# Performance work log

Measured on AMD Instinct MI355X. Metric: run time of the kernel, lower is better.

The kernel has to match this reference:

```python
import jax, jax.numpy as jnp
import numpy as np

WIN = (8, 8)
N_WIN_TOK = WIN[0] * WIN[1]  # 64
DIM = 128
HEADS = 4
HEAD_DIM = DIM // HEADS
HIDDEN = int(DIM * 0.25)
B_ = 16384


def _relative_position_index():
    ch = np.arange(WIN[0])
    cw = np.arange(WIN[1])
    coords = np.stack(np.meshgrid(ch, cw, indexing='ij'))      # (2, Wh, Ww)
    flat = coords.reshape(2, -1)                                # (2, N)
    rel = flat[:, :, None] - flat[:, None, :]                   # (2, N, N)
    rel = rel.transpose(1, 2, 0).astype(np.int32)               # (N, N, 2)
    rel[:, :, 0] += WIN[0] - 1
    rel[:, :, 1] += WIN[1] - 1
    rel[:, :, 0] *= 2 * WIN[1] - 1
    return jnp.asarray(rel.sum(-1), dtype=jnp.int32)            # (N, N)


def setup_inputs() -> dict:
    key = jax.random.key(0)
    ks = jax.random.split(key, 8)
    s_in = 1.0 / np.sqrt(DIM)
    s_h = 1.0 / np.sqrt(HIDDEN)
    return {
        'x': jax.random.normal(ks[0], (B_, N_WIN_TOK, DIM), jnp.float32),
        'rpb_table': 0.02 * jax.random.normal(ks[1], ((2 * WIN[0] - 1) * (2 * WIN[1] - 1), HEADS), jnp.float32),
        'wq': s_in * jax.random.normal(ks[2], (DIM, DIM), jnp.float32),
        'bq': jnp.zeros((DIM,), jnp.float32),
        'wkv': s_in * jax.random.normal(ks[3], (DIM, 2 * DIM), jnp.float32),
        'bkv': jnp.zeros((2 * DIM,), jnp.float32),
        'fc1_w': s_in * jax.random.normal(ks[4], (DIM, HIDDEN), jnp.float32),
        'fc1_b': jnp.zeros((HIDDEN,), jnp.float32),
        'fc2_w': s_h * jax.random.normal(ks[5], (HIDDEN, DIM), jnp.float32),
        'fc2_b': jnp.zeros((DIM,), jnp.float32),
        'rel_idx': _relative_position_index(),
    }


def reference(x, rpb_table, wq, bq, wkv, bkv, fc1_w, fc1_b, fc2_w, fc2_b, rel_idx):
    B, N, C = x.shape
    scale = HEAD_DIM ** -0.5
    # qkv projections (Uformer LinearProjection): q from to_q, k/v from to_kv
    q = (x @ wq + bq).reshape(B, N, HEADS, HEAD_DIM).transpose(0, 2, 1, 3)   # (B,h,N,d)
    kv = (x @ wkv + bkv).reshape(B, N, 2, HEADS, HEAD_DIM)
    k = kv[:, :, 0].transpose(0, 2, 1, 3)                                    # (B,h,N,d)
    v = kv[:, :, 1].transpose(0, 2, 1, 3)
    attn = jnp.einsum('bhnd,bhmd->bhnm', q * scale, k)                       # (B,h,N,N)
    bias = rpb_table[rel_idx]                                                # (N,N,h)
    attn = attn + bias.transpose(2, 0, 1)[None]                              # + (1,h,N,N)
    attn = jax.nn.softmax(attn, axis=-1)
    out = jnp.einsum('bhnm,bhmd->bhnd', attn, v).transpose(0, 2, 1, 3).reshape(B, N, C)
    # Mlp proj: fc1 -> GELU -> fc2
    out = jax.nn.gelu(out @ fc1_w + fc1_b, approximate=False) @ fc2_w + fc2_b
    return out
```

## Files before the change

### kernel.cpp

```cpp
#include <hip/hip_runtime.h>
#include <hip/hip_bf16.h>
#include <math.h>

typedef __bf16 bf16x8 __attribute__((ext_vector_type(8)));
typedef __bf16 bf16x4 __attribute__((ext_vector_type(4)));
typedef float f32x4 __attribute__((ext_vector_type(4)));

static __device__ __forceinline__ f32x4 mfma16(bf16x8 a, bf16x8 b, f32x4 c) {
  return __builtin_amdgcn_mfma_f32_16x16x32_bf16(a, b, c, 0, 0, 0);
}


__global__ void wattn_prep(const float* __restrict__ wq, const float* __restrict__ bq,
                           const float* __restrict__ wkv,
                           const float* __restrict__ f1w, const float* __restrict__ f2w,
                           const float* __restrict__ rpb, const int* __restrict__ rel,
                           char* __restrict__ ws)
{
  const int idx = blockIdx.x * 256 + threadIdx.x;
  const float scale = 0.17677669529663687f;
  unsigned short* ws16 = (unsigned short*)ws;
  float* wsf = (float*)ws;

  if (idx < 2048) {
    const int lane = idx & 63, dt = (idx >> 6) & 7, kt = idx >> 9;
    const int gg = lane >> 4, cc = lane & 15;
    bf16x8 v;
#pragma unroll
    for (int i = 0; i < 8; ++i)
      v[i] = (__bf16)(wq[(kt * 32 + gg * 8 + i) * 128 + dt * 16 + cc] * scale);
    *(bf16x8*)(ws16 + idx * 8) = v;
  } else if (idx < 4096) {
    const int e = idx - 2048;
    const int lane = e & 63, dt = (e >> 6) & 7, kt = e >> 9;
    const int gg = lane >> 4, cc = lane & 15;
    bf16x8 v;
#pragma unroll
    for (int i = 0; i < 8; ++i)
      v[i] = (__bf16)(wkv[(kt * 32 + gg * 8 + i) * 256 + dt * 16 + cc]);
    *(bf16x8*)(ws16 + 16384 + e * 8) = v;
  } else if (idx < 6144) {
    const int e = idx - 4096;
    const int lane = e & 63, dt = (e >> 6) & 7, kt = e >> 9;
    const int gg = lane >> 4, cc = lane & 15;
    bf16x8 v;
#pragma unroll
    for (int i = 0; i < 8; ++i)
      v[i] = (__bf16)(wkv[(kt * 32 + gg * 8 + i) * 256 + 128 + dt * 16 + cc]);
    *(bf16x8*)(ws16 + 32768 + e * 8) = v;
  } else if (idx < 6656) {
    const int e = idx - 6144;
    const int lane = e & 63, ht = (e >> 6) & 1, kt = e >> 7;
    const int gg = lane >> 4, cc = lane & 15;
    bf16x8 v;
#pragma unroll
    for (int i = 0; i < 8; ++i)
      v[i] = (__bf16)(f1w[(kt * 32 + gg * 8 + i) * 32 + ht * 16 + cc]);
    *(bf16x8*)(ws16 + 49152 + e * 8) = v;
  } else if (idx < 7168) {
    const int e = idx - 6656;
    const int lane = e & 63, dt = e >> 6;
    const int gg = lane >> 4, cc = lane & 15;
    bf16x8 v;
#pragma unroll
    for (int i = 0; i < 8; ++i)
      v[i] = (__bf16)(f2w[(gg * 8 + i) * 128 + dt * 16 + cc]);
    *(bf16x8*)(ws16 + 53248 + e * 8) = v;
  } else if (idx < 11264) {
    const int e = idx - 7168;
    const int lane = e & 63, nt = (e >> 6) & 3, mt = (e >> 8) & 3, h = e >> 10;
    const int gg = lane >> 4, cc = lane & 15;
    const int q = nt * 16 + cc;
    f32x4 v;
#pragma unroll
    for (int r = 0; r < 4; ++r) {
      const int key = mt * 16 + gg * 4 + r;
      v[r] = rpb[rel[q * 64 + key] * 4 + h];
    }
    *(f32x4*)(wsf + 28672 + e * 4) = v;
  } else if (idx < 11392) {
    const int d = idx - 11264;
    wsf[45056 + d] = bq[d] * scale;
  }
}

__global__ __launch_bounds__(256, 2) void wattn_main(
    const float* __restrict__ x,
    const float* __restrict__ bkv,
    const float* __restrict__ f1b,
    const float* __restrict__ f2b,
    const char* __restrict__ ws,
    float* __restrict__ out)
{
  extern __shared__ char smem[];
  const int tid = threadIdx.x;
  const int w = tid >> 6;
  const int l = tid & 63;
  const int g = l >> 4;
  const int c = l & 15;
  const size_t b = blockIdx.x;

  const unsigned short* ws16 = (const unsigned short*)ws;
  const bf16x8* wqp = (const bf16x8*)(ws16);
  const bf16x8* wkp = (const bf16x8*)(ws16 + 16384);
  const bf16x8* wvp = (const bf16x8*)(ws16 + 32768);
  const bf16x8* f1p = (const bf16x8*)(ws16 + 49152);
  const bf16x8* f2p = (const bf16x8*)(ws16 + 53248);
  const f32x4* biasp = (const f32x4*)(ws16 + 57344);
  const float* bqs = (const float*)(ws16 + 90112);

  {
    const float* xg = x + b * 8192;
#pragma unroll
    for (int i = 0; i < 8; ++i) {
      const int idx = i * 256 + tid;
      f32x4 v = *((const f32x4*)xg + idx);
      const int row = idx >> 5;
      const int col = (idx & 31) << 2;
      const int addr = (((row << 8) + (col << 1))) ^ ((row & 7) << 4);
      bf16x4 p = { (__bf16)v[0], (__bf16)v[1], (__bf16)v[2], (__bf16)v[3] };
      *(bf16x4*)(smem + addr) = p;
    }
  }
  __syncthreads();

  bf16x8 xf[4];
  {
    const int row = w * 16 + c;
    const int sw = (row & 7) << 4;
#pragma unroll
    for (int kt = 0; kt < 4; ++kt)
      xf[kt] = *(const bf16x8*)(smem + (((row << 8) + kt * 64 + (g << 4)) ^ sw));
  }
  {
    const int row = w * 16 + c;
    const int sw = (row & 7) << 4;
#pragma unroll
    for (int dt = 0; dt < 8; ++dt) {
      f32x4 aq = *(const f32x4*)(bqs + dt * 16 + g * 4);
      f32x4 ak = *(const f32x4*)(bkv + dt * 16 + g * 4);
#pragma unroll
      for (int kt = 0; kt < 4; ++kt) {
        aq = mfma16(wqp[(kt * 8 + dt) * 64 + l], xf[kt], aq);
        ak = mfma16(wkp[(kt * 8 + dt) * 64 + l], xf[kt], ak);
      }
      const int addr = (((row << 8) + dt * 32 + g * 8)) ^ sw;
      bf16x4 q4 = { (__bf16)aq[0], (__bf16)aq[1], (__bf16)aq[2], (__bf16)aq[3] };
      bf16x4 k4 = { (__bf16)ak[0], (__bf16)ak[1], (__bf16)ak[2], (__bf16)ak[3] };
      *(bf16x4*)(smem + 16384 + addr) = q4;
      *(bf16x4*)(smem + 32768 + addr) = k4;
    }
  }
  {
#pragma unroll
    for (int dt = 0; dt < 8; ++dt) {
      const float bv = bkv[128 + dt * 16 + c];
      f32x4 av = { bv, bv, bv, bv };
#pragma unroll
      for (int kt = 0; kt < 4; ++kt)
        av = mfma16(xf[kt], wvp[(kt * 8 + dt) * 64 + l], av);
      const int row = dt * 16 + c;
      const int addr = (((row << 7) + w * 32 + g * 8)) ^ ((row & 7) << 4);
      bf16x4 v4 = { (__bf16)av[0], (__bf16)av[1], (__bf16)av[2], (__bf16)av[3] };
      *(bf16x4*)(smem + 49152 + addr) = v4;
    }
  }
  __syncthreads();

  bf16x8 ka[4], qb[4];
#pragma unroll
  for (int t4 = 0; t4 < 4; ++t4) {
    const int row = t4 * 16 + c;
    const int addr = (((row << 8) + w * 64 + (g << 4))) ^ ((row & 7) << 4);
    ka[t4] = *(const bf16x8*)(smem + 32768 + addr);
    qb[t4] = *(const bf16x8*)(smem + 16384 + addr);
  }
  f32x4 s[4][4];
#pragma unroll
  for (int mt = 0; mt < 4; ++mt)
#pragma unroll
    for (int nt = 0; nt < 4; ++nt)
      s[mt][nt] = mfma16(ka[mt], qb[nt], biasp[((w * 4 + mt) * 4 + nt) * 64 + l]);
  __syncthreads();

  float rinv[4];
#pragma unroll
  for (int nt = 0; nt < 4; ++nt) {
    float m = s[0][nt][0];
#pragma unroll
    for (int mt = 0; mt < 4; ++mt)
#pragma unroll
      for (int r = 0; r < 4; ++r)
        m = fmaxf(m, s[mt][nt][r]);
    m = fmaxf(m, __shfl_xor(m, 16, 64));
    m = fmaxf(m, __shfl_xor(m, 32, 64));
    float sum = 0.f;
#pragma unroll
    for (int mt = 0; mt < 4; ++mt)
#pragma unroll
      for (int r = 0; r < 4; ++r) {
        const float e = __expf(s[mt][nt][r] - m);
        s[mt][nt][r] = e;
        sum += e;
      }
    sum += __shfl_xor(sum, 16, 64);
    sum += __shfl_xor(sum, 32, 64);
    rinv[nt] = 1.0f / sum;
  }

  const int pbase = (w < 2) ? (w * 8192) : (32768 + (w - 2) * 8192);
#pragma unroll
  for (int nt = 0; nt < 4; ++nt) {
    const int row = nt * 16 + c;
    const int sw = (row & 7) << 4;
#pragma unroll
    for (int mt = 0; mt < 4; ++mt) {
      const int addr = (((row << 7) + mt * 32 + g * 8)) ^ sw;
      bf16x4 p4 = { (__bf16)s[mt][nt][0], (__bf16)s[mt][nt][1],
                    (__bf16)s[mt][nt][2], (__bf16)s[mt][nt][3] };
      *(bf16x4*)(smem + pbase + addr) = p4;
    }
  }

  bf16x8 va[2][2], pbf[2][4];
#pragma unroll
  for (int dt2 = 0; dt2 < 2; ++dt2)
#pragma unroll
    for (int ks = 0; ks < 2; ++ks) {
      const int row = (2 * w + dt2) * 16 + c;
      const int addr = (((row << 7) + ks * 64 + (g << 4))) ^ ((row & 7) << 4);
      va[dt2][ks] = *(const bf16x8*)(smem + 49152 + addr);
    }
#pragma unroll
  for (int ks = 0; ks < 2; ++ks)
#pragma unroll
    for (int nt = 0; nt < 4; ++nt) {
      const int row = nt * 16 + c;
      const int addr = (((row << 7) + ks * 64 + (g << 4))) ^ ((row & 7) << 4);
      pbf[ks][nt] = *(const bf16x8*)(smem + pbase + addr);
    }
#pragma unroll
  for (int nt = 0; nt < 4; ++nt) {
    const int row = nt * 16 + c;
    const int sw = (row & 7) << 4;
    const float rv = rinv[nt];
#pragma unroll
    for (int dt2 = 0; dt2 < 2; ++dt2) {
      f32x4 acc = { 0.f, 0.f, 0.f, 0.f };
      acc = mfma16(va[dt2][0], pbf[0][nt], acc);
      acc = mfma16(va[dt2][1], pbf[1][nt], acc);
      const int addr = (((row << 8) + (2 * w + dt2) * 32 + g * 8)) ^ sw;
      bf16x4 o4 = { (__bf16)(acc[0] * rv), (__bf16)(acc[1] * rv),
                    (__bf16)(acc[2] * rv), (__bf16)(acc[3] * rv) };
      *(bf16x4*)(smem + 16384 + addr) = o4;
    }
  }
  __syncthreads();

  bf16x8 ob[4];
  {
    const int row = w * 16 + c;
    const int sw = (row & 7) << 4;
#pragma unroll
    for (int kt = 0; kt < 4; ++kt)
      ob[kt] = *(const bf16x8*)(smem + 16384 + (((row << 8) + kt * 64 + (g << 4)) ^ sw));
  }
  {
    const int row = w * 16 + c;
    const int sw = (row & 7) << 4;
#pragma unroll
    for (int ht = 0; ht < 2; ++ht) {
      f32x4 ah = *(const f32x4*)(f1b + ht * 16 + g * 4);
#pragma unroll
      for (int kt = 0; kt < 4; ++kt)
        ah = mfma16(f1p[(kt * 2 + ht) * 64 + l], ob[kt], ah);
      bf16x4 h4;
#pragma unroll
      for (int r = 0; r < 4; ++r) {
        const float v = ah[r];
        h4[r] = (__bf16)(0.5f * v * (1.0f + erff(v * 0.70710678118654752f)));
      }
      *(bf16x4*)(smem + 49152 + (((row << 6) + ht * 32 + g * 8) ^ sw)) = h4;
    }
  }
  bf16x8 ha;
  {
    const int row = w * 16 + c;
    ha = *(const bf16x8*)(smem + 49152 + (((row << 6) + (g << 4)) ^ ((row & 7) << 4)));
  }
  {
    float* og = out + b * 8192 + (size_t)(w * 16) * 128;
#pragma unroll
    for (int dt = 0; dt < 8; ++dt) {
      const float bb = f2b[dt * 16 + c];
      f32x4 ay = { bb, bb, bb, bb };
      ay = mfma16(ha, f2p[dt * 64 + l], ay);
#pragma unroll
      for (int r = 0; r < 4; ++r)
        og[(g * 4 + r) * 128 + dt * 16 + c] = ay[r];
    }
  }
}

extern "C" void kernel_launch(void* const* d_in, const int* in_sizes, int n_in,
                              void* d_out, int out_size, void* d_ws, size_t ws_size,
                              hipStream_t stream) {
  const float* x    = (const float*)d_in[0];
  const float* rpb  = (const float*)d_in[1];
  const float* wq   = (const float*)d_in[2];
  const float* bq   = (const float*)d_in[3];
  const float* wkv  = (const float*)d_in[4];
  const float* bkv  = (const float*)d_in[5];
  const float* f1w  = (const float*)d_in[6];
  const float* f1b  = (const float*)d_in[7];
  const float* f2w  = (const float*)d_in[8];
  const float* f2b  = (const float*)d_in[9];
  const int*   rel  = (const int*)d_in[10];
  float* out = (float*)d_out;
  char* ws = (char*)d_ws;
  if (ws_size < 180736) return;

  const int nB = in_sizes[0] / 8192;

  wattn_prep<<<45, 256, 0, stream>>>(wq, bq, wkv, f1w, f2w, rpb, rel, ws);
  wattn_main<<<nB, 256, 65536, stream>>>(x, bkv, f1b, f2b, ws, out);
}
```

Before: 585.8 us.

## Split work per head across waves to drop syncs and shrink LDS

```diff
diff --git a/kernel.cpp b/kernel.cpp
--- a/kernel.cpp
+++ b/kernel.cpp
@@ -84,7 +84,7 @@
   }
 }
 
-__global__ __launch_bounds__(256, 2) void wattn_main(
+__global__ __launch_bounds__(256, 3) void wattn_main(
     const float* __restrict__ x,
     const float* __restrict__ bkv,
     const float* __restrict__ f1b,
@@ -99,6 +99,9 @@
   const int g = l >> 4;
   const int c = l & 15;
   const size_t b = blockIdx.x;
+  const int WB = w * 12288;
+  const int QB = WB, KB = WB + 4096, VB = WB + 8192;
+  const int PB = WB, OB = WB + 8192, HB = WB;
 
   const unsigned short* ws16 = (const unsigned short*)ws;
   const bf16x8* wqp = (const bf16x8*)(ws16);
@@ -109,71 +112,85 @@
   const f32x4* biasp = (const f32x4*)(ws16 + 57344);
   const float* bqs = (const float*)(ws16 + 90112);
 
+  bf16x8 xf[4][4];
   {
     const float* xg = x + b * 8192;
 #pragma unroll
-    for (int i = 0; i < 8; ++i) {
-      const int idx = i * 256 + tid;
-      f32x4 v = *((const f32x4*)xg + idx);
-      const int row = idx >> 5;
-      const int col = (idx & 31) << 2;
-      const int addr = (((row << 8) + (col << 1))) ^ ((row & 7) << 4);
-      bf16x4 p = { (__bf16)v[0], (__bf16)v[1], (__bf16)v[2], (__bf16)v[3] };
-      *(bf16x4*)(smem + addr) = p;
-    }
-  }
-  __syncthreads();
-
-  bf16x8 xf[4];
-  {
-    const int row = w * 16 + c;
-    const int sw = (row & 7) << 4;
-#pragma unroll
-    for (int kt = 0; kt < 4; ++kt)
-      xf[kt] = *(const bf16x8*)(smem + (((row << 8) + kt * 64 + (g << 4)) ^ sw));
-  }
-  {
-    const int row = w * 16 + c;
-    const int sw = (row & 7) << 4;
-#pragma unroll
-    for (int dt = 0; dt < 8; ++dt) {
-      f32x4 aq = *(const f32x4*)(bqs + dt * 16 + g * 4);
-      f32x4 ak = *(const f32x4*)(bkv + dt * 16 + g * 4);
+    for (int tt = 0; tt < 4; ++tt)
 #pragma unroll
       for (int kt = 0; kt < 4; ++kt) {
-        aq = mfma16(wqp[(kt * 8 + dt) * 64 + l], xf[kt], aq);
-        ak = mfma16(wkp[(kt * 8 + dt) * 64 + l], xf[kt], ak);
-      }
-      const int addr = (((row << 8) + dt * 32 + g * 8)) ^ sw;
-      bf16x4 q4 = { (__bf16)aq[0], (__bf16)aq[1], (__bf16)aq[2], (__bf16)aq[3] };
-      bf16x4 k4 = { (__bf16)ak[0], (__bf16)ak[1], (__bf16)ak[2], (__bf16)ak[3] };
-      *(bf16x4*)(smem + 16384 + addr) = q4;
-      *(bf16x4*)(smem + 32768 + addr) = k4;
-    }
-  }
-  {
-#pragma unroll
-    for (int dt = 0; dt < 8; ++dt) {
-      const float bv = bkv[128 + dt * 16 + c];
-      f32x4 av = { bv, bv, bv, bv };
-#pragma unroll
-      for (int kt = 0; kt < 4; ++kt)
-        av = mfma16(xf[kt], wvp[(kt * 8 + dt) * 64 + l], av);
-      const int row = dt * 16 + c;
-      const int addr = (((row << 7) + w * 32 + g * 8)) ^ ((row & 7) << 4);
-      bf16x4 v4 = { (__bf16)av[0], (__bf16)av[1], (__bf16)av[2], (__bf16)av[3] };
-      *(bf16x4*)(smem + 49152 + addr) = v4;
-    }
-  }
-  __syncthreads();
+        const float* p = xg + (tt * 16 + c) * 128 + kt * 32 + g * 8;
+        f32x4 u = *(const f32x4*)p;
+        f32x4 v = *(const f32x4*)(p + 4);
+        bf16x8 f = { (__bf16)u[0], (__bf16)u[1], (__bf16)u[2], (__bf16)u[3],
+                     (__bf16)v[0], (__bf16)v[1], (__bf16)v[2], (__bf16)v[3] };
+        xf[tt][kt] = f;
+      }
+  }
+
+#pragma unroll
+  for (int dt = 0; dt < 2; ++dt) {
+    const int dtg = 2 * w + dt;
+    {
+      f32x4 qa[4], kk[4];
+      const f32x4 bq4 = *(const f32x4*)(bqs + dtg * 16 + g * 4);
+      const f32x4 bk4 = *(const f32x4*)(bkv + dtg * 16 + g * 4);
+#pragma unroll
+      for (int tt = 0; tt < 4; ++tt) { qa[tt] = bq4; kk[tt] = bk4; }
+#pragma unroll
+      for (int kt = 0; kt < 4; ++kt) {
+        const bf16x8 wfq = wqp[(kt * 8 + dtg) * 64 + l];
+        const bf16x8 wfk = wkp[(kt * 8 + dtg) * 64 + l];
+#pragma unroll
+        for (int tt = 0; tt < 4; ++tt) {
+          qa[tt] = mfma16(wfq, xf[tt][kt], qa[tt]);
+          kk[tt] = mfma16(wfk, xf[tt][kt], kk[tt]);
+        }
+      }
+#pragma unroll
+      for (int tt = 0; tt < 4; ++tt) {
+        const int q = tt * 16 + c;
+        const int off = (((q >> 1) * 128 + (q & 1) * 64 + (dt * 16 + g * 4) * 2)) ^ (((q >> 1) & 7) << 4);
+        bf16x4 q4 = { (__bf16)qa[tt][0], (__bf16)qa[tt][1], (__bf16)qa[tt][2], (__bf16)qa[tt][3] };
+        bf16x4 k4 = { (__bf16)kk[tt][0], (__bf16)kk[tt][1], (__bf16)kk[tt][2], (__bf16)kk[tt][3] };
+        *(bf16x4*)(smem + QB + off) = q4;
+        *(bf16x4*)(smem + KB + off) = k4;
+      }
+    }
+    {
+      const float bv = bkv[128 + dtg * 16 + c];
+      f32x4 va4[4];
+#pragma unroll
+      for (int tt = 0; tt < 4; ++tt) va4[tt] = (f32x4){ bv, bv, bv, bv };
+#pragma unroll
+      for (int kt = 0; kt < 4; ++kt) {
+        const bf16x8 wf = wvp[(kt * 8 + dtg) * 64 + l];
+#pragma unroll
+        for (int tt = 0; tt < 4; ++tt)
+          va4[tt] = mfma16(xf[tt][kt], wf, va4[tt]);
+      }
+#pragma unroll
+      for (int tt = 0; tt < 4; ++tt) {
+        const int dloc = dt * 16 + c;
+        const int off = ((dloc * 128 + (tt * 16 + g * 4) * 2)) ^ ((dloc & 7) << 4);
+        bf16x4 v4 = { (__bf16)va4[tt][0], (__bf16)va4[tt][1], (__bf16)va4[tt][2], (__bf16)va4[tt][3] };
+        *(bf16x4*)(smem + VB + off) = v4;
+      }
+    }
+  }
 
   bf16x8 ka[4], qb[4];
 #pragma unroll
-  for (int t4 = 0; t4 < 4; ++t4) {
-    const int row = t4 * 16 + c;
-    const int addr = (((row << 8) + w * 64 + (g << 4))) ^ ((row & 7) << 4);
-    ka[t4] = *(const bf16x8*)(smem + 32768 + addr);
-    qb[t4] = *(const bf16x8*)(smem + 16384 + addr);
+  for (int mt = 0; mt < 4; ++mt) {
+    const int key = mt * 16 + c;
+    const int off = (((key >> 1) * 128 + (key & 1) * 64 + g * 16)) ^ (((key >> 1) & 7) << 4);
+    ka[mt] = *(const bf16x8*)(smem + KB + off);
+  }
+#pragma unroll
+  for (int nt = 0; nt < 4; ++nt) {
+    const int q = nt * 16 + c;
+    const int off = (((q >> 1) * 128 + (q & 1) * 64 + g * 16)) ^ (((q >> 1) & 7) << 4);
+    qb[nt] = *(const bf16x8*)(smem + QB + off);
   }
   f32x4 s[4][4];
 #pragma unroll
@@ -181,7 +198,6 @@
 #pragma unroll
     for (int nt = 0; nt < 4; ++nt)
       s[mt][nt] = mfma16(ka[mt], qb[nt], biasp[((w * 4 + mt) * 4 + nt) * 64 + l]);
-  __syncthreads();
 
   float rinv[4];
 #pragma unroll
@@ -208,17 +224,15 @@
     rinv[nt] = 1.0f / sum;
   }
 
-  const int pbase = (w < 2) ? (w * 8192) : (32768 + (w - 2) * 8192);
 #pragma unroll
   for (int nt = 0; nt < 4; ++nt) {
-    const int row = nt * 16 + c;
-    const int sw = (row & 7) << 4;
+    const int q = nt * 16 + c;
 #pragma unroll
     for (int mt = 0; mt < 4; ++mt) {
-      const int addr = (((row << 7) + mt * 32 + g * 8)) ^ sw;
+      const int off = ((q * 128 + (mt * 16 + g * 4) * 2)) ^ ((q & 7) << 4);
       bf16x4 p4 = { (__bf16)s[mt][nt][0], (__bf16)s[mt][nt][1],
                     (__bf16)s[mt][nt][2], (__bf16)s[mt][nt][3] };
-      *(bf16x4*)(smem + pbase + addr) = p4;
+      *(bf16x4*)(smem + PB + off) = p4;
     }
   }
 
@@ -227,47 +241,44 @@
   for (int dt2 = 0; dt2 < 2; ++dt2)
 #pragma unroll
     for (int ks = 0; ks < 2; ++ks) {
-      const int row = (2 * w + dt2) * 16 + c;
-      const int addr = (((row << 7) + ks * 64 + (g << 4))) ^ ((row & 7) << 4);
-      va[dt2][ks] = *(const bf16x8*)(smem + 49152 + addr);
+      const int dloc = dt2 * 16 + c;
+      const int off = ((dloc * 128 + ks * 64 + g * 16)) ^ ((dloc & 7) << 4);
+      va[dt2][ks] = *(const bf16x8*)(smem + VB + off);
     }
 #pragma unroll
   for (int ks = 0; ks < 2; ++ks)
 #pragma unroll
     for (int nt = 0; nt < 4; ++nt) {
-      const int row = nt * 16 + c;
-      const int addr = (((row << 7) + ks * 64 + (g << 4))) ^ ((row & 7) << 4);
-      pbf[ks][nt] = *(const bf16x8*)(smem + pbase + addr);
+      const int q = nt * 16 + c;
+      const int off = ((q * 128 + ks * 64 + g * 16)) ^ ((q & 7) << 4);
+      pbf[ks][nt] = *(const bf16x8*)(smem + PB + off);
     }
 #pragma unroll
   for (int nt = 0; nt < 4; ++nt) {
-    const int row = nt * 16 + c;
-    const int sw = (row & 7) << 4;
     const float rv = rinv[nt];
+    const int q = nt * 16 + c;
 #pragma unroll
     for (int dt2 = 0; dt2 < 2; ++dt2) {
       f32x4 acc = { 0.f, 0.f, 0.f, 0.f };
       acc = mfma16(va[dt2][0], pbf[0][nt], acc);
       acc = mfma16(va[dt2][1], pbf[1][nt], acc);
-      const int addr = (((row << 8) + (2 * w + dt2) * 32 + g * 8)) ^ sw;
+      const int off = (((q >> 1) * 128 + (q & 1) * 64 + (dt2 * 16 + g * 4) * 2)) ^ (((q >> 1) & 7) << 4);
       bf16x4 o4 = { (__bf16)(acc[0] * rv), (__bf16)(acc[1] * rv),
                     (__bf16)(acc[2] * rv), (__bf16)(acc[3] * rv) };
-      *(bf16x4*)(smem + 16384 + addr) = o4;
-    }
-  }
+      *(bf16x4*)(smem + OB + off) = o4;
+    }
+  }
+
   __syncthreads();
 
   bf16x8 ob[4];
+#pragma unroll
+  for (int kt = 0; kt < 4; ++kt) {
+    const int t = w * 16 + c;
+    const int off = (((t >> 1) * 128 + (t & 1) * 64 + g * 16)) ^ (((t >> 1) & 7) << 4);
+    ob[kt] = *(const bf16x8*)(smem + kt * 12288 + 8192 + off);
+  }
   {
-    const int row = w * 16 + c;
-    const int sw = (row & 7) << 4;
-#pragma unroll
-    for (int kt = 0; kt < 4; ++kt)
-      ob[kt] = *(const bf16x8*)(smem + 16384 + (((row << 8) + kt * 64 + (g << 4)) ^ sw));
-  }
-  {
-    const int row = w * 16 + c;
-    const int sw = (row & 7) << 4;
 #pragma unroll
     for (int ht = 0; ht < 2; ++ht) {
       f32x4 ah = *(const f32x4*)(f1b + ht * 16 + g * 4);
@@ -280,13 +291,14 @@
         const float v = ah[r];
         h4[r] = (__bf16)(0.5f * v * (1.0f + erff(v * 0.70710678118654752f)));
       }
-      *(bf16x4*)(smem + 49152 + (((row << 6) + ht * 32 + g * 8) ^ sw)) = h4;
+      const int off = (((c >> 1) * 128 + (c & 1) * 64 + (ht * 16 + g * 4) * 2)) ^ (((c >> 1) & 7) << 4);
+      *(bf16x4*)(smem + HB + off) = h4;
     }
   }
   bf16x8 ha;
   {
-    const int row = w * 16 + c;
-    ha = *(const bf16x8*)(smem + 49152 + (((row << 6) + (g << 4)) ^ ((row & 7) << 4)));
+    const int off = (((c >> 1) * 128 + (c & 1) * 64 + g * 16)) ^ (((c >> 1) & 7) << 4);
+    ha = *(const bf16x8*)(smem + HB + off);
   }
   {
     float* og = out + b * 8192 + (size_t)(w * 16) * 128;
@@ -323,5 +335,5 @@
   const int nB = in_sizes[0] / 8192;
 
   wattn_prep<<<45, 256, 0, stream>>>(wq, bq, wkv, f1w, f2w, rpb, rel, ws);
-  wattn_main<<<nB, 256, 65536, stream>>>(x, bkv, f1b, f2b, ws, out);
+  wattn_main<<<nB, 256, 49152, stream>>>(x, bkv, f1b, f2b, ws, out);
 }
```

Measured after the change: 587.8 us. Within noise of the previous version (+0.3%).
